# Kernel tuning notes

Hardware: AMD Instinct MI355X
Metric: run time of the kernel (lower is better)

## Reference

```python
import jax, jax.numpy as jnp
import numpy as np

B, H, W = 512, 15, 15
DF, DP, DV, DD = 64, 32, 64, 32
PM = 16
NUM_LINE = 442503  # get_total_num_line_encoding(11)


def fake_quant(x, scale=128., num_bits=8, floor=False):
    qmin = float(-(2 ** (num_bits - 1)))
    qmax = float(2 ** (num_bits - 1) - 1)
    xs = jnp.clip(x * scale, qmin, qmax)
    q = jnp.floor(xs) if floor else jnp.round(xs)
    q = xs + jax.lax.stop_gradient(q - xs)  # straight-through estimator
    return q / scale


def qw(w):  # LinearBlock quant=True weight: int8 at scale 128
    return fake_quant(w, 128., 8)


def qb(b):  # LinearBlock quant=True bias: int32 at scale 128*128
    return fake_quant(b, 128. * 128., 32)


def setup_inputs() -> dict:
    key = jax.random.key(0)
    ks = jax.random.split(key, 24)
    n = lambda k, shape, s=0.1: jax.random.normal(k, shape, dtype=jnp.float32) * s
    return {
        'line_encoding': jax.random.randint(ks[0], (B, 4, H, W), 0, NUM_LINE, dtype=jnp.int32),
        'emb': n(ks[1], (NUM_LINE, DF), 0.5),
        'dw_w': n(ks[2], (DD, 3, 3)),
        'dw_b': n(ks[3], (DD,)),
        'pw1_w': n(ks[4], (DP * 2, DF)), 'pw1_b': n(ks[5], (DP * 2,)),
        'pw2_w': n(ks[6], (PM * DP + PM, DP * 2)), 'pw2_b': n(ks[7], (PM * DP + PM,)),
        'pout_w': n(ks[8], (PM,), 0.2), 'pout_b': n(ks[9], (1,), 0.2),
        'star_up1_w': n(ks[10], (4, DV, DF)), 'star_up1_b': n(ks[11], (4, DV)),
        'star_up2_w': n(ks[12], (4, DV, DF)), 'star_up2_b': n(ks[13], (4, DV)),
        'star_down_w': n(ks[14], (4, DV, DV)), 'star_down_b': n(ks[15], (4, DV)),
        'vl1_w': n(ks[16], (DV, DF + 4 * DV)), 'vl1_b': n(ks[17], (DV,)),
        'vl2_w': n(ks[18], (DV, DV)), 'vl2_b': n(ks[19], (DV,)),
        'vl3_w': n(ks[20], (3, DV)), 'vl3_b': n(ks[21], (3,)),
    }


def _star(x, w1, b1, w2, b2, w3, b3):
    # x: [B,R,DF]; weights [R,DV,DF] (per-region parameter gather)
    x1 = jnp.einsum('brc,rdc->brd', x, qw(w1)) + qb(b1)[None]
    x2 = jnp.einsum('brc,rdc->brd', x, qw(w2)) + qb(b2)[None]
    h = jax.nn.relu(x1) * x2  # star operation
    return jnp.einsum('brc,rdc->brd', h, qw(w3)) + qb(b3)[None]


def _forward(line_encoding, emb, dw_w, dw_b, pw1_w, pw1_b, pw2_w, pw2_b,
             pout_w, pout_b, star_up1_w, star_up1_b, star_up2_w, star_up2_b,
             star_down_w, star_down_b, vl1_w, vl1_b, vl2_w, vl2_b, vl3_w, vl3_b):
    # ---- feature: embedding gather + quant + direction mean ----
    f = emb[line_encoding]                       # [B,4,H,W,DF]
    f = jnp.clip(f, -16., 16.)
    f = fake_quant(f, 32., 16)
    f = jax.nn.relu(jnp.mean(f, axis=1))         # [B,H,W,DF]
    f = jnp.transpose(f, (0, 3, 1, 2))           # [B,DF,H,W]
    # ---- depthwise 3x3 conv, quant='pixel-dwconv-floor' ----
    x = fake_quant(f[:, :DD] * 4., 128., 16)
    wq = fake_quant(dw_w, 65536., 16)
    bq = fake_quant(dw_b, 128., 16)
    xp = jnp.pad(x, ((0, 0), (0, 0), (1, 1), (1, 1)))
    pat = jnp.stack([xp[:, :, dy:dy + H, dx:dx + W]
                     for dy in range(3) for dx in range(3)], axis=2)  # [B,DD,9,H,W]
    prod = fake_quant(pat * wq.reshape(1, DD, 9, 1, 1), 128., 32, floor=True)
    conv = jax.nn.relu(prod.sum(axis=2) + bq.reshape(1, DD, 1, 1))
    feat_dw = fake_quant(conv, 128., 16)
    feat_dir = fake_quant(f[:, DD:], 128., 16)
    feature = jnp.concatenate([feat_dw, feat_dir], axis=1)  # [B,DF,H,W]
    # ---- global and 3x3 regional sums ----
    feature_sum = fake_quant(feature.sum(axis=(2, 3)) / 256., 128., 32, floor=True)
    Hs = [0, H // 3 + (H % 3 == 2), H // 3 * 2 + (H % 3 > 0), H]
    Ws = [0, W // 3 + (W % 3 == 2), W // 3 * 2 + (W % 3 > 0), W]
    regions = jnp.stack([feature[:, :, Hs[i]:Hs[i + 1], Ws[j]:Ws[j + 1]].sum(axis=(2, 3))
                         for i in range(3) for j in range(3)], axis=1)  # [B,9,DF]
    regions = fake_quant(regions / 32., 128., 32, floor=True)
    # ---- policy: dynamic per-sample pointwise conv ----
    h = jax.nn.relu(feature_sum @ qw(pw1_w).T + qb(pw1_b))
    o = h @ qw(pw2_w).T + qb(pw2_b)                         # [B, PM*DP+PM]
    pw = fake_quant(o[:, :PM * DP], 128. * 128., 16, floor=True).reshape(-1, PM, DP)
    pin = fake_quant(feature[:, :DP], 128., 16)             # [B,DP,H,W]
    pol = jnp.einsum('bchw,bic->bihw', pin, pw)             # grouped conv, groups=B
    pbias = o[:, PM * DP:].reshape(-1, PM, 1, 1)
    pol = jax.nn.relu(pol + pbias)
    policy = jnp.einsum('bihw,i->bhw', pol, pout_w)[:, None] + pout_b[0]  # [B,1,H,W]
    # ---- value: corner/edge/center star blocks over 9 regions ----
    idx = jnp.array([0, 1, 0, 1, 2, 1, 0, 1, 0])  # 0=corner,1=edge,2=center
    v = _star(regions, star_up1_w[idx], star_up1_b[idx], star_up2_w[idx],
              star_up2_b[idx], star_down_w[idx], star_down_b[idx])  # [B,9,DV]
    fq8 = lambda t: fake_quant(t, 128., 8, floor=True)
    def avg4(a, b, c, d):
        a, b, c, d = fq8(a), fq8(b), fq8(c), fq8(d)
        ab = fq8((a + b + 1. / 128.) / 2.)
        cd = fq8((c + d + 1. / 128.) / 2.)
        return fq8((ab + cd + 1. / 128.) / 2.)
    quads = jnp.stack([avg4(v[:, 0], v[:, 1], v[:, 3], v[:, 4]),
                       avg4(v[:, 1], v[:, 2], v[:, 4], v[:, 5]),
                       avg4(v[:, 3], v[:, 4], v[:, 6], v[:, 7]),
                       avg4(v[:, 4], v[:, 5], v[:, 7], v[:, 8])], axis=1)  # [B,4,DV]
    qidx = jnp.array([3, 3, 3, 3])  # value_quad shared across quadrants
    vq = _star(quads, star_up1_w[qidx], star_up1_b[qidx], star_up2_w[qidx],
               star_up2_b[qidx], star_down_w[qidx], star_down_b[qidx])  # [B,4,DV]
    value = jnp.concatenate([feature_sum, vq.reshape(vq.shape[0], -1)], axis=1)  # [B,320]
    value = jax.nn.relu(value @ qw(vl1_w).T + qb(vl1_b))
    value = jax.nn.relu(value @ qw(vl2_w).T + qb(vl2_b))
    value = value @ qw(vl3_w).T + qb(vl3_b)                 # [B,3]
    return value, policy


def reference(line_encoding, emb, dw_w, dw_b, pw1_w, pw1_b, pw2_w, pw2_b,
              pout_w, pout_b, star_up1_w, star_up1_b, star_up2_w, star_up2_b,
              star_down_w, star_down_b, vl1_w, vl1_b, vl2_w, vl2_b, vl3_w, vl3_b):
    return _forward(line_encoding, emb, dw_w, dw_b, pw1_w, pw1_b, pw2_w, pw2_b,
                    pout_w, pout_b, star_up1_w, star_up1_b, star_up2_w, star_up2_b,
                    star_down_w, star_down_b, vl1_w, vl1_b, vl2_w, vl2_b, vl3_w, vl3_b)
```

## Files before the change

### kernel.cpp

```cpp
#include <hip/hip_runtime.h>

#define NPOS 225
#define FSTR 226

#define OFF_PW1Q 0
#define OFF_PW2Q 4096
#define OFF_SU1Q 37888
#define OFF_SU2Q 54272
#define OFF_SDQ  70656
#define OFF_VL1Q 87040
#define OFF_VL2Q 107520
#define OFF_VL3Q 111616
#define OFF_PW1B 111808
#define OFF_PW2B 111872
#define OFF_SU1B 112400
#define OFF_SU2B 112656
#define OFF_SDB  112912
#define OFF_VL1B 113168
#define OFF_VL2B 113232
#define OFF_VL3B 113296
#define OFF_DWW  113300
#define OFF_DWB  113588
#define WS_TOTAL 113620

__device__ __forceinline__ float qw8(float w) {
  return rintf(fminf(fmaxf(w * 128.f, -128.f), 127.f)) * 0.0078125f;
}
__device__ __forceinline__ float qb32(float b) {
  return rintf(b * 16384.f) * 6.103515625e-05f;
}
__device__ __forceinline__ float fq8f(float v) {
  return floorf(fminf(fmaxf(v * 128.f, -128.f), 127.f)) * 0.0078125f;
}
__device__ __forceinline__ float qd32(float v) {
  return rintf(fminf(fmaxf(v, -16.f), 16.f) * 32.f);
}

__global__ __launch_bounds__(256)
void nnue_prep(const float* __restrict__ pw1_w, const float* __restrict__ pw1_b,
               const float* __restrict__ pw2_w, const float* __restrict__ pw2_b,
               const float* __restrict__ su1w,  const float* __restrict__ su1b,
               const float* __restrict__ su2w,  const float* __restrict__ su2b,
               const float* __restrict__ sdw,   const float* __restrict__ sdb,
               const float* __restrict__ vl1w,  const float* __restrict__ vl1b,
               const float* __restrict__ vl2w,  const float* __restrict__ vl2b,
               const float* __restrict__ vl3w,  const float* __restrict__ vl3b,
               const float* __restrict__ dw_w,  const float* __restrict__ dw_b,
               float* __restrict__ wsf, int* __restrict__ wsi)
{
  const int i = blockIdx.x * 256 + threadIdx.x;
  if (i < 111808) {
    const float* src; int off;
    if      (i < 4096)   { src = pw1_w; off = 0; }
    else if (i < 37888)  { src = pw2_w; off = 4096; }
    else if (i < 54272)  { src = su1w;  off = 37888; }
    else if (i < 70656)  { src = su2w;  off = 54272; }
    else if (i < 87040)  { src = sdw;   off = 70656; }
    else if (i < 107520) { src = vl1w;  off = 87040; }
    else if (i < 111616) { src = vl2w;  off = 107520; }
    else                 { src = vl3w;  off = 111616; }
    wsf[i] = qw8(src[i - off]);
  } else if (i < 113299) {
    const int j = i - 111808;
    const float* src; int off;
    if      (j < 64)   { src = pw1_b; off = 0; }
    else if (j < 592)  { src = pw2_b; off = 64; }
    else if (j < 848)  { src = su1b;  off = 592; }
    else if (j < 1104) { src = su2b;  off = 848; }
    else if (j < 1360) { src = sdb;   off = 1104; }
    else if (j < 1424) { src = vl1b;  off = 1360; }
    else if (j < 1488) { src = vl2b;  off = 1424; }
    else               { src = vl3b;  off = 1488; }
    wsf[i] = qb32(src[j - off]);
  } else if (i >= 113300 && i < 113588) {
    wsi[i] = (int)rintf(fminf(fmaxf(dw_w[i - 113300] * 65536.f, -32768.f), 32767.f));
  } else if (i >= 113588 && i < 113620) {
    wsi[i] = (int)rintf(fminf(fmaxf(dw_b[i - 113588] * 128.f, -32768.f), 32767.f));
  }
}

__global__ __launch_bounds__(512, 2)
void nnue_main(const int* __restrict__ line, const float* __restrict__ emb,
               const float* __restrict__ pout_w, const float* __restrict__ pout_b,
               const float* __restrict__ wsf, const int* __restrict__ wsi,
               float* __restrict__ out)
{
  __shared__ unsigned short fbuf[64 * FSTR];
  __shared__ unsigned short fbuf2[32 * FSTR];
  __shared__ int sle[900];
  __shared__ float sreg[576];
  __shared__ float sfsum[64];
  __shared__ float shh[64];
  __shared__ float sobuf[528];
  __shared__ float spwq[512];
  __shared__ float hstar[576];
  __shared__ float vstar[576];
  __shared__ float squads[256];
  __shared__ float shq[256];
  __shared__ float svq[256];
  __shared__ float sv1[64];
  __shared__ float sv2[64];

  const int tid  = threadIdx.x;
  const int b    = blockIdx.x;
  const int wid  = __builtin_amdgcn_readfirstlane(tid >> 6);
  const int lane = tid & 63;
  const int* le  = line + b * 4 * NPOS;

  for (int i = tid; i < 900; i += 512) sle[i] = le[i];
  __syncthreads();

  {
    const int s = (wid * NPOS) >> 3;
    const int e = ((wid + 1) * NPOS) >> 3;
    for (int p0 = s; p0 < e; p0 += 8) {
      int sidx[32];
#pragma unroll
      for (int j = 0; j < 8; ++j) {
        int pp = p0 + j; pp = (pp < e) ? pp : (e - 1);
#pragma unroll
        for (int d = 0; d < 4; ++d)
          sidx[j * 4 + d] = __builtin_amdgcn_readfirstlane(sle[d * NPOS + pp]);
      }
      float vv[32];
#pragma unroll
      for (int t = 0; t < 32; ++t)
        vv[t] = emb[(unsigned)(sidx[t] * 64 + lane)];
#pragma unroll
      for (int j = 0; j < 8; ++j) {
        int pp = p0 + j; pp = (pp < e) ? pp : (e - 1);
        float sm = qd32(vv[4 * j]) + qd32(vv[4 * j + 1]) + qd32(vv[4 * j + 2]) + qd32(vv[4 * j + 3]);
        fbuf[lane * FSTR + pp] = (unsigned short)fmaxf(sm, 0.f);
      }
    }
  }
  __syncthreads();

  {
    const int cc = tid >> 4;
    const int pg = tid & 15;
    int w9[9];
#pragma unroll
    for (int t = 0; t < 9; ++t) w9[t] = wsi[OFF_DWW + cc * 9 + t];
    const int bqi = wsi[OFF_DWB + cc];
    const unsigned short* frow = &fbuf[cc * FSTR];
#pragma unroll
    for (int k = 0; k < 15; ++k) {
      const int p = pg + 16 * k;
      if (p < NPOS) {
        const int y0 = (p * 2185) >> 15;
        const int x0 = p - y0 * 15;
        const int ym = (y0 > 0), yp = (y0 < 14), xm = (x0 > 0), xp = (x0 < 14);
        int acc = 0;
#pragma unroll
        for (int dy = 0; dy < 3; ++dy) {
          const int vy = (dy == 0) ? ym : ((dy == 2) ? yp : 1);
#pragma unroll
          for (int dx = 0; dx < 3; ++dx) {
            const int vx = (dx == 0) ? xm : ((dx == 2) ? xp : 1);
            int q = p + (dy - 1) * 15 + (dx - 1);
            q = (q < 0) ? 0 : ((q > 224) ? 224 : q);
            int kk = frow[q];
            kk = (vy && vx) ? kk : 0;
            acc += (kk * 4 * w9[dy * 3 + dx]) >> 16;
          }
        }
        int res = acc + bqi;
        res = res < 0 ? 0 : res;
        res = res > 32767 ? 32767 : res;
        fbuf2[cc * FSTR + p] = (unsigned short)res;
      }
    }
  }
  __syncthreads();

  {
    int* sregKi = (int*)sreg;
    for (int task = tid; task < 576; task += 512) {
      const int r = task >> 6, c = task & 63;
      const int rh = (r * 11) >> 5;
      const int rw = r - rh * 3;
      const unsigned short* base = (c < 32) ? &fbuf2[c * FSTR] : &fbuf[c * FSTR];
      const unsigned short* fr = base + rh * 75 + rw * 5;
      int K = 0;
#pragma unroll
      for (int y = 0; y < 5; ++y)
#pragma unroll
        for (int x = 0; x < 5; ++x) K += fr[y * 15 + x];
      sregKi[task] = K;
    }
  }
  __syncthreads();
  if (tid < 64) {
    int* sregKi = (int*)sreg;
    int Ks[9], tot = 0;
#pragma unroll
    for (int r = 0; r < 9; ++r) { Ks[r] = sregKi[r * 64 + tid]; tot += Ks[r]; }
#pragma unroll
    for (int r = 0; r < 9; ++r) sreg[r * 64 + tid] = (float)(Ks[r] >> 5) * 0.0078125f;
    sfsum[tid] = (float)(tot >> 8) * 0.0078125f;
  }
  __syncthreads();

  if (tid < 64) {
    const float4* wr = (const float4*)(wsf + OFF_PW1Q + tid * 64);
    float acc = 0.f;
#pragma unroll
    for (int c4 = 0; c4 < 16; ++c4) {
      float4 w = wr[c4];
      acc += sfsum[c4 * 4 + 0] * w.x + sfsum[c4 * 4 + 1] * w.y
           + sfsum[c4 * 4 + 2] * w.z + sfsum[c4 * 4 + 3] * w.w;
    }
    shh[tid] = fmaxf(acc + wsf[OFF_PW1B + tid], 0.f);
  } else if (tid >= 256) {
    const int g = (tid >> 6) - 4;
    const int d = tid & 63;
    int ty, rA, rB, rC, rD;
    if (g == 0)      { ty = 0; rA = 0; rB = 2; rC = 6; rD = 8; }
    else if (g == 1) { ty = 1; rA = 1; rB = 3; rC = 5; rD = 7; }
    else             { ty = 2; rA = 4; rB = 4; rC = 4; rD = 4; }
    if (g < 3) {
      const float4* w1r = (const float4*)(wsf + OFF_SU1Q + ty * 4096 + d * 64);
      const float4* w2r = (const float4*)(wsf + OFF_SU2Q + ty * 4096 + d * 64);
      float aA1 = 0, aB1 = 0, aC1 = 0, aD1 = 0, aA2 = 0, aB2 = 0, aC2 = 0, aD2 = 0;
#pragma unroll 4
      for (int c4 = 0; c4 < 16; ++c4) {
        float4 w1 = w1r[c4], w2 = w2r[c4];
        float q1[4] = {w1.x, w1.y, w1.z, w1.w};
        float q2[4] = {w2.x, w2.y, w2.z, w2.w};
#pragma unroll
        for (int u = 0; u < 4; ++u) {
          const int c = c4 * 4 + u;
          float xA = sreg[rA * 64 + c], xB = sreg[rB * 64 + c];
          float xC = sreg[rC * 64 + c], xD = sreg[rD * 64 + c];
          aA1 += xA * q1[u]; aB1 += xB * q1[u]; aC1 += xC * q1[u]; aD1 += xD * q1[u];
          aA2 += xA * q2[u]; aB2 += xB * q2[u]; aC2 += xC * q2[u]; aD2 += xD * q2[u];
        }
      }
      const float bb1 = wsf[OFF_SU1B + ty * 64 + d];
      const float bb2 = wsf[OFF_SU2B + ty * 64 + d];
      hstar[rA * 64 + d] = fmaxf(aA1 + bb1, 0.f) * (aA2 + bb2);
      hstar[rB * 64 + d] = fmaxf(aB1 + bb1, 0.f) * (aB2 + bb2);
      hstar[rC * 64 + d] = fmaxf(aC1 + bb1, 0.f) * (aC2 + bb2);
      hstar[rD * 64 + d] = fmaxf(aD1 + bb1, 0.f) * (aD2 + bb2);
    }
  }
  __syncthreads();

  if (tid < 256) {
    for (int j = tid; j < 528; j += 256) {
      const float4* wr = (const float4*)(wsf + OFF_PW2Q + j * 64);
      float acc = 0.f;
#pragma unroll
      for (int c4 = 0; c4 < 16; ++c4) {
        float4 w = wr[c4];
        acc += shh[c4 * 4 + 0] * w.x + shh[c4 * 4 + 1] * w.y
             + shh[c4 * 4 + 2] * w.z + shh[c4 * 4 + 3] * w.w;
      }
      acc += wsf[OFF_PW2B + j];
      sobuf[j] = acc;
      if (j < 512)
        spwq[j] = floorf(fminf(fmaxf(acc * 16384.f, -32768.f), 32767.f)) * 6.103515625e-05f;
    }
  } else {
    const int g = (tid >> 6) - 4;
    const int d = tid & 63;
    int ty, rA, rB, rC, rD;
    if (g == 0)      { ty = 0; rA = 0; rB = 2; rC = 6; rD = 8; }
    else if (g == 1) { ty = 1; rA = 1; rB = 3; rC = 5; rD = 7; }
    else             { ty = 2; rA = 4; rB = 4; rC = 4; rD = 4; }
    if (g < 3) {
      const float4* wdr = (const float4*)(wsf + OFF_SDQ + ty * 4096 + d * 64);
      float dA = 0, dB = 0, dC = 0, dD = 0;
#pragma unroll 4
      for (int c4 = 0; c4 < 16; ++c4) {
        float4 w = wdr[c4];
        float q[4] = {w.x, w.y, w.z, w.w};
#pragma unroll
        for (int u = 0; u < 4; ++u) {
          const int c = c4 * 4 + u;
          dA += hstar[rA * 64 + c] * q[u]; dB += hstar[rB * 64 + c] * q[u];
          dC += hstar[rC * 64 + c] * q[u]; dD += hstar[rD * 64 + c] * q[u];
        }
      }
      const float bd = wsf[OFF_SDB + ty * 64 + d];
      vstar[rA * 64 + d] = dA + bd;
      vstar[rB * 64 + d] = dB + bd;
      vstar[rC * 64 + d] = dC + bd;
      vstar[rD * 64 + d] = dD + bd;
    }
  }
  __syncthreads();

  if (tid < NPOS) {
    float pinv[32];
#pragma unroll
    for (int c = 0; c < 32; ++c) pinv[c] = (float)fbuf2[c * FSTR + tid] * 0.0078125f;
    float acc = 0.f;
#pragma unroll
    for (int i = 0; i < 16; ++i) {
      float s = 0.f;
#pragma unroll
      for (int c = 0; c < 32; ++c) s += pinv[c] * spwq[i * 32 + c];
      s = fmaxf(s + sobuf[512 + i], 0.f);
      acc += s * pout_w[i];
    }
    out[1536 + b * NPOS + tid] = acc + pout_b[0];
  } else if (tid >= 256) {
    const int g = (tid >> 6) - 4;
    const int d = tid & 63;
    int r0, r1, r2v, r3v;
    if (g == 0)      { r0 = 0; r1 = 1; r2v = 3; r3v = 4; }
    else if (g == 1) { r0 = 1; r1 = 2; r2v = 4; r3v = 5; }
    else if (g == 2) { r0 = 3; r1 = 4; r2v = 6; r3v = 7; }
    else             { r0 = 4; r1 = 5; r2v = 7; r3v = 8; }
    float a  = fq8f(vstar[r0 * 64 + d]);
    float bb = fq8f(vstar[r1 * 64 + d]);
    float cc = fq8f(vstar[r2v * 64 + d]);
    float dd = fq8f(vstar[r3v * 64 + d]);
    float ab = fq8f((a + bb + 0.0078125f) * 0.5f);
    float cd = fq8f((cc + dd + 0.0078125f) * 0.5f);
    squads[g * 64 + d] = fq8f((ab + cd + 0.0078125f) * 0.5f);
  }
  __syncthreads();

  if (tid >= 256) {
    const int g = (tid >> 6) - 4;
    const int d = tid & 63;
    const float4* w1r = (const float4*)(wsf + OFF_SU1Q + 3 * 4096 + d * 64);
    const float4* w2r = (const float4*)(wsf + OFF_SU2Q + 3 * 4096 + d * 64);
    float a1 = 0.f, a2 = 0.f;
#pragma unroll 4
    for (int c4 = 0; c4 < 16; ++c4) {
      float4 w1 = w1r[c4], w2 = w2r[c4];
      float xq0 = squads[g * 64 + c4 * 4 + 0], xq1 = squads[g * 64 + c4 * 4 + 1];
      float xq2 = squads[g * 64 + c4 * 4 + 2], xq3 = squads[g * 64 + c4 * 4 + 3];
      a1 += xq0 * w1.x + xq1 * w1.y + xq2 * w1.z + xq3 * w1.w;
      a2 += xq0 * w2.x + xq1 * w2.y + xq2 * w2.z + xq3 * w2.w;
    }
    shq[g * 64 + d] = fmaxf(a1 + wsf[OFF_SU1B + 192 + d], 0.f) * (a2 + wsf[OFF_SU2B + 192 + d]);
  }
  __syncthreads();

  if (tid >= 256) {
    const int g = (tid >> 6) - 4;
    const int d = tid & 63;
    const float4* wdr = (const float4*)(wsf + OFF_SDQ + 3 * 4096 + d * 64);
    float ad = 0.f;
#pragma unroll 4
    for (int c4 = 0; c4 < 16; ++c4) {
      float4 w = wdr[c4];
      ad += shq[g * 64 + c4 * 4 + 0] * w.x + shq[g * 64 + c4 * 4 + 1] * w.y
          + shq[g * 64 + c4 * 4 + 2] * w.z + shq[g * 64 + c4 * 4 + 3] * w.w;
    }
    svq[g * 64 + d] = ad + wsf[OFF_SDB + 192 + d];
  }
  __syncthreads();

  if (tid < 64) {
    const float4* wr = (const float4*)(wsf + OFF_VL1Q + tid * 320);
    float acc = 0.f;
#pragma unroll 4
    for (int k4 = 0; k4 < 16; ++k4) {
      float4 w = wr[k4];
      acc += sfsum[k4 * 4 + 0] * w.x + sfsum[k4 * 4 + 1] * w.y
           + sfsum[k4 * 4 + 2] * w.z + sfsum[k4 * 4 + 3] * w.w;
    }
#pragma unroll 4
    for (int k4 = 16; k4 < 80; ++k4) {
      float4 w = wr[k4];
      const int base = k4 * 4 - 64;
      acc += svq[base + 0] * w.x + svq[base + 1] * w.y
           + svq[base + 2] * w.z + svq[base + 3] * w.w;
    }
    sv1[tid] = fmaxf(acc + wsf[OFF_VL1B + tid], 0.f);
  }
  __syncthreads();
  if (tid < 64) {
    const float4* wr = (const float4*)(wsf + OFF_VL2Q + tid * 64);
    float acc = 0.f;
#pragma unroll 4
    for (int k4 = 0; k4 < 16; ++k4) {
      float4 w = wr[k4];
      acc += sv1[k4 * 4 + 0] * w.x + sv1[k4 * 4 + 1] * w.y
           + sv1[k4 * 4 + 2] * w.z + sv1[k4 * 4 + 3] * w.w;
    }
    sv2[tid] = fmaxf(acc + wsf[OFF_VL2B + tid], 0.f);
  }
  __syncthreads();
  if (tid < 3) {
    const float* wr = wsf + OFF_VL3Q + tid * 64;
    float acc = 0.f;
#pragma unroll
    for (int k = 0; k < 64; ++k) acc += sv2[k] * wr[k];
    out[b * 3 + tid] = acc + wsf[OFF_VL3B + tid];
  }
}

extern "C" void kernel_launch(void* const* d_in, const int* in_sizes, int n_in,
                              void* d_out, int out_size, void* d_ws, size_t ws_size,
                              hipStream_t stream) {
  (void)in_sizes; (void)n_in; (void)out_size; (void)ws_size;
  float* wsf = (float*)d_ws;
  int*   wsi = (int*)d_ws;
  nnue_prep<<<(WS_TOTAL + 255) / 256, 256, 0, stream>>>(
      (const float*)d_in[4],  (const float*)d_in[5],
      (const float*)d_in[6],  (const float*)d_in[7],
      (const float*)d_in[10], (const float*)d_in[11],
      (const float*)d_in[12], (const float*)d_in[13],
      (const float*)d_in[14], (const float*)d_in[15],
      (const float*)d_in[16], (const float*)d_in[17],
      (const float*)d_in[18], (const float*)d_in[19],
      (const float*)d_in[20], (const float*)d_in[21],
      (const float*)d_in[2],  (const float*)d_in[3],
      wsf, wsi);
  nnue_main<<<512, 512, 0, stream>>>(
      (const int*)d_in[0], (const float*)d_in[1],
      (const float*)d_in[8], (const float*)d_in[9],
      wsf, wsi, (float*)d_out);
}
```

Measured before the change: 271.7 us.

## Split embedding gather into separate wide kernel feeding a smaller-LDS tail kernel

The embedding gather moves out of the monolithic per-board kernel into its own kernel with a 15x512 grid of small blocks, which write quantized features to a workspace buffer in position-major layout. A tail kernel then reloads each board's features into LDS, reuses the feature buffer as scratch for later stages, and runs the depthwise conv and MLP heads at higher occupancy. The intent is to expose more parallelism to hide the latency of the random embedding reads. The cost is an extra global round trip of about 15 MB of intermediates and one more launch. The old fused kernel stays as a fallback when the workspace is too small.

```diff
diff --git a/kernel.cpp b/kernel.cpp
--- a/kernel.cpp
+++ b/kernel.cpp
@@ -2,6 +2,7 @@
 
 #define NPOS 225
 #define FSTR 226
+#define FINSTR 66
 
 #define OFF_PW1Q 0
 #define OFF_PW2Q 4096
@@ -22,6 +23,8 @@
 #define OFF_DWW  113300
 #define OFF_DWB  113588
 #define WS_TOTAL 113620
+#define F_BYTE_OFF 454480
+#define F_BYTES  (512u*225u*64u*2u)
 
 __device__ __forceinline__ float qw8(float w) {
   return rintf(fminf(fmaxf(w * 128.f, -128.f), 127.f)) * 0.0078125f;
@@ -79,11 +82,352 @@
   }
 }
 
-__global__ __launch_bounds__(512, 2)
-void nnue_main(const int* __restrict__ line, const float* __restrict__ emb,
+__global__ __launch_bounds__(256, 8)
+void nnue_gather(const int* __restrict__ line, const float* __restrict__ emb,
+                 unsigned short* __restrict__ fout)
+{
+  const int b    = blockIdx.y;
+  const int w    = threadIdx.x >> 6;
+  const int lane = threadIdx.x & 63;
+  const int p0   = blockIdx.x * 16 + w * 4;
+  const int* le  = line + b * 900;
+  int sidx[16];
+#pragma unroll
+  for (int j = 0; j < 4; ++j) {
+    int pp = p0 + j; pp = pp < NPOS ? pp : NPOS - 1;
+#pragma unroll
+    for (int d = 0; d < 4; ++d)
+      sidx[j * 4 + d] = __builtin_amdgcn_readfirstlane(le[d * NPOS + pp]);
+  }
+  float vv[16];
+#pragma unroll
+  for (int t = 0; t < 16; ++t)
+    vv[t] = emb[(unsigned)(sidx[t] * 64 + lane)];
+  unsigned short* fb = fout + b * 14400;
+#pragma unroll
+  for (int j = 0; j < 4; ++j) {
+    const int pp = p0 + j;
+    if (pp < NPOS) {
+      float sm = qd32(vv[4 * j]) + qd32(vv[4 * j + 1]) + qd32(vv[4 * j + 2]) + qd32(vv[4 * j + 3]);
+      fb[pp * 64 + lane] = (unsigned short)fmaxf(sm, 0.f);
+    }
+  }
+}
+
+__global__ __launch_bounds__(512, 6)
+void nnue_tail(const unsigned short* __restrict__ fsrc,
                const float* __restrict__ pout_w, const float* __restrict__ pout_b,
                const float* __restrict__ wsf, const int* __restrict__ wsi,
                float* __restrict__ out)
+{
+  __shared__ float finf[7426];
+  __shared__ unsigned short fbuf2[32 * FSTR];
+  __shared__ float sreg[576];
+  __shared__ float sfsum[64];
+  unsigned short* fin = (unsigned short*)finf;
+  float* tail = finf;
+#define SHH(i)    tail[(i)]
+#define SOBUF(i)  tail[64 + (i)]
+#define SPWQ(i)   tail[592 + (i)]
+#define HSTAR(i)  tail[1104 + (i)]
+#define VSTAR(i)  tail[1680 + (i)]
+#define SQUADS(i) tail[2256 + (i)]
+#define SHQ(i)    tail[2512 + (i)]
+#define SVQ(i)    tail[2768 + (i)]
+#define SV1(i)    tail[3024 + (i)]
+#define SV2(i)    tail[3088 + (i)]
+
+  const int tid = threadIdx.x;
+  const int b   = blockIdx.x;
+
+  {
+    const unsigned int* src = (const unsigned int*)(fsrc + b * 14400);
+    for (int l = tid; l < 7200; l += 512) {
+      unsigned int v = src[l];
+      const int p = l >> 5, cc = (l & 31) << 1;
+      *(unsigned int*)&fin[p * FINSTR + cc] = v;
+    }
+  }
+  __syncthreads();
+
+  if (tid < 450) {
+    int p, c0;
+    if (tid < 225) { p = tid; c0 = 0; } else { p = tid - 225; c0 = 16; }
+    const int y0 = (p * 2185) >> 15;
+    const int x0 = p - y0 * 15;
+    const int ym = (y0 > 0), yp = (y0 < 14), xm = (x0 > 0), xp = (x0 < 14);
+    int qv[9], vm[9];
+#pragma unroll
+    for (int dy = 0; dy < 3; ++dy) {
+      const int vy = (dy == 0) ? ym : ((dy == 2) ? yp : 1);
+#pragma unroll
+      for (int dx = 0; dx < 3; ++dx) {
+        const int vx = (dx == 0) ? xm : ((dx == 2) ? xp : 1);
+        int q = p + (dy - 1) * 15 + (dx - 1);
+        q = q < 0 ? 0 : (q > 224 ? 224 : q);
+        qv[dy * 3 + dx] = q * FINSTR;
+        vm[dy * 3 + dx] = vy && vx;
+      }
+    }
+    for (int c = c0; c < c0 + 16; ++c) {
+      const int wb = OFF_DWW + c * 9;
+      int acc = 0;
+#pragma unroll
+      for (int t = 0; t < 9; ++t) {
+        int kk = vm[t] ? (int)fin[qv[t] + c] : 0;
+        acc += (kk * 4 * wsi[wb + t]) >> 16;
+      }
+      int res = acc + wsi[OFF_DWB + c];
+      res = res < 0 ? 0 : (res > 32767 ? 32767 : res);
+      fbuf2[c * FSTR + p] = (unsigned short)res;
+    }
+  }
+  __syncthreads();
+
+  {
+    int* sregKi = (int*)sreg;
+    for (int task = tid; task < 576; task += 512) {
+      const int r = task >> 6, c = task & 63;
+      const int rh = (r * 11) >> 5, rw = r - rh * 3;
+      int K = 0;
+      if (c < 32) {
+        const unsigned short* fr = &fbuf2[c * FSTR + rh * 75 + rw * 5];
+#pragma unroll
+        for (int y = 0; y < 5; ++y)
+#pragma unroll
+          for (int x = 0; x < 5; ++x) K += fr[y * 15 + x];
+      } else {
+        const unsigned short* fr = &fin[(rh * 75 + rw * 5) * FINSTR + c];
+#pragma unroll
+        for (int y = 0; y < 5; ++y)
+#pragma unroll
+          for (int x = 0; x < 5; ++x) K += fr[(y * 15 + x) * FINSTR];
+      }
+      sregKi[task] = K;
+    }
+  }
+  __syncthreads();
+  if (tid < 64) {
+    int* sregKi = (int*)sreg;
+    int Ks[9], tot = 0;
+#pragma unroll
+    for (int r = 0; r < 9; ++r) { Ks[r] = sregKi[r * 64 + tid]; tot += Ks[r]; }
+#pragma unroll
+    for (int r = 0; r < 9; ++r) sreg[r * 64 + tid] = (float)(Ks[r] >> 5) * 0.0078125f;
+    sfsum[tid] = (float)(tot >> 8) * 0.0078125f;
+  }
+  __syncthreads();
+
+  if (tid < 64) {
+    const float4* wr = (const float4*)(wsf + OFF_PW1Q + tid * 64);
+    float acc = 0.f;
+#pragma unroll
+    for (int c4 = 0; c4 < 16; ++c4) {
+      float4 w = wr[c4];
+      acc += sfsum[c4 * 4 + 0] * w.x + sfsum[c4 * 4 + 1] * w.y
+           + sfsum[c4 * 4 + 2] * w.z + sfsum[c4 * 4 + 3] * w.w;
+    }
+    SHH(tid) = fmaxf(acc + wsf[OFF_PW1B + tid], 0.f);
+  } else if (tid >= 256) {
+    const int g = (tid >> 6) - 4;
+    const int d = tid & 63;
+    int ty, rA, rB, rC, rD;
+    if (g == 0)      { ty = 0; rA = 0; rB = 2; rC = 6; rD = 8; }
+    else if (g == 1) { ty = 1; rA = 1; rB = 3; rC = 5; rD = 7; }
+    else             { ty = 2; rA = 4; rB = 4; rC = 4; rD = 4; }
+    if (g < 3) {
+      const float4* w1r = (const float4*)(wsf + OFF_SU1Q + ty * 4096 + d * 64);
+      const float4* w2r = (const float4*)(wsf + OFF_SU2Q + ty * 4096 + d * 64);
+      float aA1 = 0, aB1 = 0, aC1 = 0, aD1 = 0, aA2 = 0, aB2 = 0, aC2 = 0, aD2 = 0;
+#pragma unroll 4
+      for (int c4 = 0; c4 < 16; ++c4) {
+        float4 w1 = w1r[c4], w2 = w2r[c4];
+        float q1[4] = {w1.x, w1.y, w1.z, w1.w};
+        float q2[4] = {w2.x, w2.y, w2.z, w2.w};
+#pragma unroll
+        for (int u = 0; u < 4; ++u) {
+          const int c = c4 * 4 + u;
+          float xA = sreg[rA * 64 + c], xB = sreg[rB * 64 + c];
+          float xC = sreg[rC * 64 + c], xD = sreg[rD * 64 + c];
+          aA1 += xA * q1[u]; aB1 += xB * q1[u]; aC1 += xC * q1[u]; aD1 += xD * q1[u];
+          aA2 += xA * q2[u]; aB2 += xB * q2[u]; aC2 += xC * q2[u]; aD2 += xD * q2[u];
+        }
+      }
+      const float bb1 = wsf[OFF_SU1B + ty * 64 + d];
+      const float bb2 = wsf[OFF_SU2B + ty * 64 + d];
+      HSTAR(rA * 64 + d) = fmaxf(aA1 + bb1, 0.f) * (aA2 + bb2);
+      HSTAR(rB * 64 + d) = fmaxf(aB1 + bb1, 0.f) * (aB2 + bb2);
+      HSTAR(rC * 64 + d) = fmaxf(aC1 + bb1, 0.f) * (aC2 + bb2);
+      HSTAR(rD * 64 + d) = fmaxf(aD1 + bb1, 0.f) * (aD2 + bb2);
+    }
+  }
+  __syncthreads();
+
+  if (tid < 256) {
+    for (int j = tid; j < 528; j += 256) {
+      const float4* wr = (const float4*)(wsf + OFF_PW2Q + j * 64);
+      float acc = 0.f;
+#pragma unroll
+      for (int c4 = 0; c4 < 16; ++c4) {
+        float4 w = wr[c4];
+        acc += SHH(c4 * 4 + 0) * w.x + SHH(c4 * 4 + 1) * w.y
+             + SHH(c4 * 4 + 2) * w.z + SHH(c4 * 4 + 3) * w.w;
+      }
+      acc += wsf[OFF_PW2B + j];
+      SOBUF(j) = acc;
+      if (j < 512)
+        SPWQ(j) = floorf(fminf(fmaxf(acc * 16384.f, -32768.f), 32767.f)) * 6.103515625e-05f;
+    }
+  } else {
+    const int g = (tid >> 6) - 4;
+    const int d = tid & 63;
+    int ty, rA, rB, rC, rD;
+    if (g == 0)      { ty = 0; rA = 0; rB = 2; rC = 6; rD = 8; }
+    else if (g == 1) { ty = 1; rA = 1; rB = 3; rC = 5; rD = 7; }
+    else             { ty = 2; rA = 4; rB = 4; rC = 4; rD = 4; }
+    if (g < 3) {
+      const float4* wdr = (const float4*)(wsf + OFF_SDQ + ty * 4096 + d * 64);
+      float dA = 0, dB = 0, dC = 0, dD = 0;
+#pragma unroll 4
+      for (int c4 = 0; c4 < 16; ++c4) {
+        float4 w = wdr[c4];
+        float q[4] = {w.x, w.y, w.z, w.w};
+#pragma unroll
+        for (int u = 0; u < 4; ++u) {
+          const int c = c4 * 4 + u;
+          dA += HSTAR(rA * 64 + c) * q[u]; dB += HSTAR(rB * 64 + c) * q[u];
+          dC += HSTAR(rC * 64 + c) * q[u]; dD += HSTAR(rD * 64 + c) * q[u];
+        }
+      }
+      const float bd = wsf[OFF_SDB + ty * 64 + d];
+      VSTAR(rA * 64 + d) = dA + bd;
+      VSTAR(rB * 64 + d) = dB + bd;
+      VSTAR(rC * 64 + d) = dC + bd;
+      VSTAR(rD * 64 + d) = dD + bd;
+    }
+  }
+  __syncthreads();
+
+  if (tid < NPOS) {
+    float pinv[32];
+#pragma unroll
+    for (int c = 0; c < 32; ++c) pinv[c] = (float)fbuf2[c * FSTR + tid] * 0.0078125f;
+    float acc = 0.f;
+#pragma unroll
+    for (int i = 0; i < 16; ++i) {
+      float s = 0.f;
+#pragma unroll
+      for (int c = 0; c < 32; ++c) s += pinv[c] * SPWQ(i * 32 + c);
+      s = fmaxf(s + SOBUF(512 + i), 0.f);
+      acc += s * pout_w[i];
+    }
+    out[1536 + b * NPOS + tid] = acc + pout_b[0];
+  } else if (tid >= 256) {
+    const int g = (tid >> 6) - 4;
+    const int d = tid & 63;
+    int r0, r1, r2v, r3v;
+    if (g == 0)      { r0 = 0; r1 = 1; r2v = 3; r3v = 4; }
+    else if (g == 1) { r0 = 1; r1 = 2; r2v = 4; r3v = 5; }
+    else if (g == 2) { r0 = 3; r1 = 4; r2v = 6; r3v = 7; }
+    else             { r0 = 4; r1 = 5; r2v = 7; r3v = 8; }
+    float a  = fq8f(VSTAR(r0 * 64 + d));
+    float bb = fq8f(VSTAR(r1 * 64 + d));
+    float cc = fq8f(VSTAR(r2v * 64 + d));
+    float dd = fq8f(VSTAR(r3v * 64 + d));
+    float ab = fq8f((a + bb + 0.0078125f) * 0.5f);
+    float cd = fq8f((cc + dd + 0.0078125f) * 0.5f);
+    SQUADS(g * 64 + d) = fq8f((ab + cd + 0.0078125f) * 0.5f);
+  }
+  __syncthreads();
+
+  if (tid >= 256) {
+    const int g = (tid >> 6) - 4;
+    const int d = tid & 63;
+    const float4* w1r = (const float4*)(wsf + OFF_SU1Q + 3 * 4096 + d * 64);
+    const float4* w2r = (const float4*)(wsf + OFF_SU2Q + 3 * 4096 + d * 64);
+    float a1 = 0.f, a2 = 0.f;
+#pragma unroll 4
+    for (int c4 = 0; c4 < 16; ++c4) {
+      float4 w1 = w1r[c4], w2 = w2r[c4];
+      float xq0 = SQUADS(g * 64 + c4 * 4 + 0), xq1 = SQUADS(g * 64 + c4 * 4 + 1);
+      float xq2 = SQUADS(g * 64 + c4 * 4 + 2), xq3 = SQUADS(g * 64 + c4 * 4 + 3);
+      a1 += xq0 * w1.x + xq1 * w1.y + xq2 * w1.z + xq3 * w1.w;
+      a2 += xq0 * w2.x + xq1 * w2.y + xq2 * w2.z + xq3 * w2.w;
+    }
+    SHQ(g * 64 + d) = fmaxf(a1 + wsf[OFF_SU1B + 192 + d], 0.f) * (a2 + wsf[OFF_SU2B + 192 + d]);
+  }
+  __syncthreads();
+
+  if (tid >= 256) {
+    const int g = (tid >> 6) - 4;
+    const int d = tid & 63;
+    const float4* wdr = (const float4*)(wsf + OFF_SDQ + 3 * 4096 + d * 64);
+    float ad = 0.f;
+#pragma unroll 4
+    for (int c4 = 0; c4 < 16; ++c4) {
+      float4 w = wdr[c4];
+      ad += SHQ(g * 64 + c4 * 4 + 0) * w.x + SHQ(g * 64 + c4 * 4 + 1) * w.y
+          + SHQ(g * 64 + c4 * 4 + 2) * w.z + SHQ(g * 64 + c4 * 4 + 3) * w.w;
+    }
+    SVQ(g * 64 + d) = ad + wsf[OFF_SDB + 192 + d];
+  }
+  __syncthreads();
+
+  if (tid < 64) {
+    const float4* wr = (const float4*)(wsf + OFF_VL1Q + tid * 320);
+    float acc = 0.f;
+#pragma unroll 4
+    for (int k4 = 0; k4 < 16; ++k4) {
+      float4 w = wr[k4];
+      acc += sfsum[k4 * 4 + 0] * w.x + sfsum[k4 * 4 + 1] * w.y
+           + sfsum[k4 * 4 + 2] * w.z + sfsum[k4 * 4 + 3] * w.w;
+    }
+#pragma unroll 4
+    for (int k4 = 16; k4 < 80; ++k4) {
+      float4 w = wr[k4];
+      const int base = k4 * 4 - 64;
+      acc += SVQ(base + 0) * w.x + SVQ(base + 1) * w.y
+           + SVQ(base + 2) * w.z + SVQ(base + 3) * w.w;
+    }
+    SV1(tid) = fmaxf(acc + wsf[OFF_VL1B + tid], 0.f);
+  }
+  __syncthreads();
+  if (tid < 64) {
+    const float4* wr = (const float4*)(wsf + OFF_VL2Q + tid * 64);
+    float acc = 0.f;
+#pragma unroll 4
+    for (int k4 = 0; k4 < 16; ++k4) {
+      float4 w = wr[k4];
+      acc += SV1(k4 * 4 + 0) * w.x + SV1(k4 * 4 + 1) * w.y
+           + SV1(k4 * 4 + 2) * w.z + SV1(k4 * 4 + 3) * w.w;
+    }
+    SV2(tid) = fmaxf(acc + wsf[OFF_VL2B + tid], 0.f);
+  }
+  __syncthreads();
+  if (tid < 3) {
+    const float* wr = wsf + OFF_VL3Q + tid * 64;
+    float acc = 0.f;
+#pragma unroll
+    for (int k = 0; k < 64; ++k) acc += SV2(k) * wr[k];
+    out[b * 3 + tid] = acc + wsf[OFF_VL3B + tid];
+  }
+#undef SHH
+#undef SOBUF
+#undef SPWQ
+#undef HSTAR
+#undef VSTAR
+#undef SQUADS
+#undef SHQ
+#undef SVQ
+#undef SV1
+#undef SV2
+}
+
+__global__ __launch_bounds__(512, 4)
+void nnue_fused(const int* __restrict__ line, const float* __restrict__ emb,
+                const float* __restrict__ pout_w, const float* __restrict__ pout_b,
+                const float* __restrict__ wsf, const int* __restrict__ wsi,
+                float* __restrict__ out)
 {
   __shared__ unsigned short fbuf[64 * FSTR];
   __shared__ unsigned short fbuf2[32 * FSTR];
@@ -100,16 +444,13 @@
   __shared__ float svq[256];
   __shared__ float sv1[64];
   __shared__ float sv2[64];
-
   const int tid  = threadIdx.x;
   const int b    = blockIdx.x;
   const int wid  = __builtin_amdgcn_readfirstlane(tid >> 6);
   const int lane = tid & 63;
   const int* le  = line + b * 4 * NPOS;
-
   for (int i = tid; i < 900; i += 512) sle[i] = le[i];
   __syncthreads();
-
   {
     const int s = (wid * NPOS) >> 3;
     const int e = ((wid + 1) * NPOS) >> 3;
@@ -124,8 +465,7 @@
       }
       float vv[32];
 #pragma unroll
-      for (int t = 0; t < 32; ++t)
-        vv[t] = emb[(unsigned)(sidx[t] * 64 + lane)];
+      for (int t = 0; t < 32; ++t) vv[t] = emb[(unsigned)(sidx[t] * 64 + lane)];
 #pragma unroll
       for (int j = 0; j < 8; ++j) {
         int pp = p0 + j; pp = (pp < e) ? pp : (e - 1);
@@ -135,7 +475,6 @@
     }
   }
   __syncthreads();
-
   {
     const int cc = tid >> 4;
     const int pg = tid & 15;
@@ -173,7 +512,6 @@
     }
   }
   __syncthreads();
-
   {
     int* sregKi = (int*)sreg;
     for (int task = tid; task < 576; task += 512) {
@@ -201,7 +539,6 @@
     sfsum[tid] = (float)(tot >> 8) * 0.0078125f;
   }
   __syncthreads();
-
   if (tid < 64) {
     const float4* wr = (const float4*)(wsf + OFF_PW1Q + tid * 64);
     float acc = 0.f;
@@ -246,7 +583,6 @@
     }
   }
   __syncthreads();
-
   if (tid < 256) {
     for (int j = tid; j < 528; j += 256) {
       const float4* wr = (const float4*)(wsf + OFF_PW2Q + j * 64);
@@ -291,7 +627,6 @@
     }
   }
   __syncthreads();
-
   if (tid < NPOS) {
     float pinv[32];
 #pragma unroll
@@ -323,7 +658,6 @@
     squads[g * 64 + d] = fq8f((ab + cd + 0.0078125f) * 0.5f);
   }
   __syncthreads();
-
   if (tid >= 256) {
     const int g = (tid >> 6) - 4;
     const int d = tid & 63;
@@ -341,7 +675,6 @@
     shq[g * 64 + d] = fmaxf(a1 + wsf[OFF_SU1B + 192 + d], 0.f) * (a2 + wsf[OFF_SU2B + 192 + d]);
   }
   __syncthreads();
-
   if (tid >= 256) {
     const int g = (tid >> 6) - 4;
     const int d = tid & 63;
@@ -356,7 +689,6 @@
     svq[g * 64 + d] = ad + wsf[OFF_SDB + 192 + d];
   }
   __syncthreads();
-
   if (tid < 64) {
     const float4* wr = (const float4*)(wsf + OFF_VL1Q + tid * 320);
     float acc = 0.f;
@@ -400,7 +732,7 @@
 extern "C" void kernel_launch(void* const* d_in, const int* in_sizes, int n_in,
                               void* d_out, int out_size, void* d_ws, size_t ws_size,
                               hipStream_t stream) {
-  (void)in_sizes; (void)n_in; (void)out_size; (void)ws_size;
+  (void)in_sizes; (void)n_in; (void)out_size;
   float* wsf = (float*)d_ws;
   int*   wsi = (int*)d_ws;
   nnue_prep<<<(WS_TOTAL + 255) / 256, 256, 0, stream>>>(
@@ -414,8 +746,17 @@
       (const float*)d_in[20], (const float*)d_in[21],
       (const float*)d_in[2],  (const float*)d_in[3],
       wsf, wsi);
-  nnue_main<<<512, 512, 0, stream>>>(
-      (const int*)d_in[0], (const float*)d_in[1],
-      (const float*)d_in[8], (const float*)d_in[9],
-      wsf, wsi, (float*)d_out);
-}
+  const size_t need = (size_t)F_BYTE_OFF + (size_t)F_BYTES;
+  if (ws_size >= need) {
+    unsigned short* f = (unsigned short*)((char*)d_ws + F_BYTE_OFF);
+    nnue_gather<<<dim3(15, 512), 256, 0, stream>>>(
+        (const int*)d_in[0], (const float*)d_in[1], f);
+    nnue_tail<<<512, 512, 0, stream>>>(
+        f, (const float*)d_in[8], (const float*)d_in[9], wsf, wsi, (float*)d_out);
+  } else {
+    nnue_fused<<<512, 512, 0, stream>>>(
+        (const int*)d_in[0], (const float*)d_in[1],
+        (const float*)d_in[8], (const float*)d_in[9],
+        wsf, wsi, (float*)d_out);
+  }
+}
```

After: 282.7 us. 4.1% more time.
